# Kernel tuning notes

Hardware: AMD Instinct MI355X
Metric: run time of the kernel (lower is better)

## Reference

```python
import jax, jax.numpy as jnp
import numpy as np

N, DIM, HEADS, DHEAD = 4096, 1024, 16, 64
INNER = HEADS * DHEAD


def setup_inputs() -> dict:
    key = jax.random.key(0)
    ks = jax.random.split(key, 6)
    s_in = 1.0 / np.sqrt(DIM)
    s_inner = 1.0 / np.sqrt(INNER)
    return {
        "x": jax.random.normal(ks[0], (N, DIM), dtype=jnp.float32),
        # weights stored as (in, out) so y = x @ W
        "Wq": jax.random.uniform(ks[1], (DIM, INNER), jnp.float32, -s_in, s_in),
        "Wk": jax.random.uniform(ks[2], (DIM, INNER), jnp.float32, -s_in, s_in),
        "Wv": jax.random.uniform(ks[3], (DIM, INNER), jnp.float32, -s_in, s_in),
        "Wo": jax.random.uniform(ks[4], (INNER, DIM), jnp.float32, -s_inner, s_inner),
        "bo": jax.random.uniform(ks[5], (DIM,), jnp.float32, -s_inner, s_inner),
    }


def reference(x, Wq, Wk, Wv, Wo, bo):
    scale = DHEAD ** -0.5
    # [n, h, d] -> [h, n, d]
    q = (x @ Wq).reshape(N, HEADS, DHEAD).transpose(1, 0, 2)
    k = (x @ Wk).reshape(N, HEADS, DHEAD).transpose(1, 0, 2)
    v = (x @ Wv).reshape(N, HEADS, DHEAD).transpose(1, 0, 2)
    dots = jnp.einsum("hnd,hmd->hnm", q, k) * scale  # [h, n, n]
    attn = jax.nn.softmax(dots, axis=-1)
    out = jnp.einsum("hnm,hmd->hnd", attn, v)  # [h, n, d]
    out = out.transpose(1, 0, 2).reshape(N, INNER)
    return out @ Wo + bo
```

## Files before the change

kernel.cpp:

```cpp
#include <hip/hip_runtime.h>
#include <cstdint>
#include <cstddef>

typedef _Float16 f16;
typedef _Float16 f16x8 __attribute__((ext_vector_type(8)));
typedef _Float16 f16x4 __attribute__((ext_vector_type(4)));
typedef __fp16 fp16x2 __attribute__((ext_vector_type(2)));
typedef float floatx4 __attribute__((ext_vector_type(4)));
typedef float floatx16 __attribute__((ext_vector_type(16)));

constexpr int SEQ = 4096;
constexpr int DIM = 1024;
constexpr int NHEAD = 16;
constexpr int DH = 64;

#define QSCALE 0.18033688011112042f

__device__ __forceinline__ void async16(void* lds, const void* g) {
  __builtin_amdgcn_global_load_lds(
      (__attribute__((address_space(1))) void*)g,
      (__attribute__((address_space(3))) void*)lds, 16, 0, 0);
}

__device__ __forceinline__ uint32_t pk2(float a, float b) {
  union { fp16x2 h; uint32_t u; } c;
  c.h = __builtin_amdgcn_cvt_pkrtz(a, b);
  return c.u;
}

__device__ __forceinline__ float dot2acc(uint32_t packed, float acc) {
#if __has_builtin(__builtin_amdgcn_fdot2)
  union { uint32_t u; fp16x2 h; } c; c.u = packed;
  fp16x2 one2; one2.x = (__fp16)1.0f; one2.y = (__fp16)1.0f;
  return __builtin_amdgcn_fdot2(c.h, one2, acc, false);
#else
  union { uint32_t u; fp16x2 h; } c; c.u = packed;
  return acc + (float)c.h.x + (float)c.h.y;
#endif
}

__global__ void prep(const float* __restrict__ x, const float* __restrict__ w0,
                     const float* __restrict__ w1, const float* __restrict__ w2,
                     const float* __restrict__ w3, f16* __restrict__ xh,
                     f16* __restrict__ o0, f16* __restrict__ o1,
                     f16* __restrict__ o2, f16* __restrict__ o3) {
  int z = blockIdx.z;
  if (z == 4) {
    int blk = blockIdx.y * 32 + blockIdx.x;
    int tid = threadIdx.y * 32 + threadIdx.x;
    int base = (blk * 256 + tid) * 4;
#pragma unroll
    for (int c = 0; c < 4; ++c) {
      int i = base + c * (SEQ * DIM / 4);
      float4 v = *(const float4*)(x + i);
      f16x4 o;
      o.x = (f16)v.x; o.y = (f16)v.y; o.z = (f16)v.z; o.w = (f16)v.w;
      *(f16x4*)(xh + i) = o;
    }
    return;
  }
  __shared__ float tile[32][33];
  const float* W = (z == 0) ? w0 : (z == 1) ? w1 : (z == 2) ? w2 : w3;
  f16* O = (z == 0) ? o0 : (z == 1) ? o1 : (z == 2) ? o2 : o3;
  int tx = threadIdx.x, ty = threadIdx.y;
  int xc = blockIdx.x * 32 + tx;
  for (int i = ty; i < 32; i += 8)
    tile[i][tx] = W[(size_t)(blockIdx.y * 32 + i) * DIM + xc];
  __syncthreads();
  int xo = blockIdx.y * 32 + tx;
  for (int i = ty; i < 32; i += 8)
    O[(size_t)(blockIdx.x * 32 + i) * DIM + xo] = (f16)tile[tx][i];
}

__global__ __launch_bounds__(256, 2) void gemm_qkv(
    const f16* __restrict__ xh, const f16* __restrict__ wqt,
    const f16* __restrict__ wkt, const f16* __restrict__ wvt,
    f16* __restrict__ q_ws, f16* __restrict__ k_ws, f16* __restrict__ vt_ws) {
  __shared__ f16 smem[36864];
  const int tid = threadIdx.x;
  const int lane = tid & 63, l16 = lane & 15, quad = lane >> 4;
  const int w = tid >> 6, wr = w >> 1, wc = w & 1;
  const int m0 = blockIdx.x * 128, n0 = blockIdx.y * 256;
  const int z = blockIdx.z;
  const f16* Bt = (z == 0) ? wqt : (z == 1) ? wkt : wvt;

  floatx4 acc[4][8];
#pragma unroll
  for (int mt = 0; mt < 4; ++mt)
#pragma unroll
    for (int nt = 0; nt < 8; ++nt) acc[mt][nt] = (floatx4){0.f, 0.f, 0.f, 0.f};

#define QKV_STAGE(t_, buf_)                                                    \
  {                                                                            \
    int k0_ = (t_) * 32;                                                       \
    _Pragma("unroll")                                                          \
    for (int rnd = 0; rnd < 2; ++rnd) {                                        \
      int e = (rnd * 256 + tid) * 8;                                           \
      int cb = e >> 10, r = (e >> 3) & 127;                                    \
      async16((buf_) + e, xh + (size_t)(m0 + r) * DIM + k0_ + cb * 8);         \
    }                                                                          \
    _Pragma("unroll")                                                          \
    for (int rnd = 0; rnd < 4; ++rnd) {                                        \
      int e = (rnd * 256 + tid) * 8;                                           \
      int cb = e >> 11, r = (e >> 3) & 255;                                    \
      async16((buf_) + 4096 + e, Bt + (size_t)(n0 + r) * DIM + k0_ + cb * 8);  \
    }                                                                          \
  }

  QKV_STAGE(0, smem);
  QKV_STAGE(1, smem + 12288);
  for (int t = 0; t < 32; ++t) {
    f16* cur = smem + (t % 3) * 12288;
    if (t + 2 < 32) {
      QKV_STAGE(t + 2, smem + ((t + 2) % 3) * 12288);
      asm volatile("s_waitcnt vmcnt(12)" ::: "memory");
    } else if (t + 1 < 32) {
      asm volatile("s_waitcnt vmcnt(6)" ::: "memory");
    } else {
      asm volatile("s_waitcnt vmcnt(0)" ::: "memory");
    }
    __builtin_amdgcn_s_barrier();
    asm volatile("" ::: "memory");
    const f16* a_lds = cur;
    const f16* b_lds = cur + 4096;
    f16x8 af[4], bq[8];
#pragma unroll
    for (int mt = 0; mt < 4; ++mt)
      af[mt] = *(const f16x8*)(a_lds + quad * 1024 + (wr * 64 + mt * 16 + l16) * 8);
#pragma unroll
    for (int nt = 0; nt < 8; ++nt)
      bq[nt] = *(const f16x8*)(b_lds + quad * 2048 + (wc * 128 + nt * 16 + l16) * 8);
#pragma unroll
    for (int mt = 0; mt < 4; ++mt)
#pragma unroll
      for (int nt = 0; nt < 8; ++nt)
        acc[mt][nt] = __builtin_amdgcn_mfma_f32_16x16x32_f16(af[mt], bq[nt], acc[mt][nt], 0, 0, 0);
    asm volatile("" ::: "memory");
    __builtin_amdgcn_s_barrier();
  }
#undef QKV_STAGE

  if (z < 2) {
#pragma unroll
    for (int mt = 0; mt < 4; ++mt)
#pragma unroll
      for (int nt = 0; nt < 8; ++nt)
#pragma unroll
        for (int r = 0; r < 4; ++r) {
          int m = m0 + wr * 64 + mt * 16 + quad * 4 + r;
          int c = n0 + wc * 128 + nt * 16 + l16;
          float v = acc[mt][nt][r];
          if (z == 0)
            q_ws[(size_t)((c >> 6) * SEQ + m) * DH + (c & 63)] = (f16)(v * QSCALE);
          else
            k_ws[(size_t)((c >> 6) * SEQ + m) * DH + (c & 63)] = (f16)v;
        }
  } else {
#pragma unroll
    for (int ch = 0; ch < 2; ++ch) {
      if (wc == ch) {
#pragma unroll
        for (int mt = 0; mt < 4; ++mt)
#pragma unroll
          for (int nt = 0; nt < 8; ++nt)
#pragma unroll
            for (int r = 0; r < 4; ++r) {
              int cl = nt * 16 + l16;
              int ml = wr * 64 + mt * 16 + quad * 4 + r;
              smem[cl * 132 + ml] = (f16)acc[mt][nt][r];
            }
      }
      __syncthreads();
#pragma unroll
      for (int it = 0; it < 8; ++it) {
        int idx = it * 256 + tid;
        int cl = idx >> 4, mp = (idx & 15) * 8;
        f16x4 lo = *(const f16x4*)(smem + cl * 132 + mp);
        f16x4 hi4 = *(const f16x4*)(smem + cl * 132 + mp + 4);
        f16x8 v8;
#pragma unroll
        for (int j = 0; j < 4; ++j) { v8[j] = lo[j]; v8[4 + j] = hi4[j]; }
        *(f16x8*)(vt_ws + (size_t)(n0 + ch * 128 + cl) * SEQ + m0 + mp) = v8;
      }
      __syncthreads();
    }
  }
}

__global__ __launch_bounds__(256, 4) void attn_kernel(
    const f16* __restrict__ qg, const f16* __restrict__ kg,
    const f16* __restrict__ vtg, f16* __restrict__ og) {
  __shared__ f16 smem[16384];

  const int tid = threadIdx.x;
  const int w = tid >> 6, lane = tid & 63, l32 = lane & 31;
  const int hi = lane >> 5;

  const int pid = blockIdx.x + 32 * blockIdx.y;
  const int vid = (pid & 7) * 64 + (pid >> 3);
  const int qt = vid & 31, h = vid >> 5;

  const int q0 = qt * 128 + w * 32;

  f16x8 qf[4];
#pragma unroll
  for (int kf = 0; kf < 4; ++kf)
    qf[kf] = *(const f16x8*)(qg + (size_t)(h * SEQ + q0 + l32) * DH + kf * 16 + hi * 8);

  floatx16 oacc[2];
  oacc[0] = (floatx16)0.f; oacc[1] = (floatx16)0.f;
  float ssa = 0.f, ssb = 0.f;

  const f16* kg_h = kg + (size_t)h * SEQ * DH;
  const f16* vt_h = vtg + (size_t)h * DH * SEQ;
  constexpr int NT = SEQ / 64;

  {
#pragma unroll
    for (int rnd = 0; rnd < 2; ++rnd) {
      int e = (rnd * 256 + tid) * 8;
      int cb = e >> 9, r = (e >> 3) & 63;
      async16(smem + e, kg_h + (size_t)r * DH + cb * 8);
      async16(smem + 4096 + e, vt_h + (size_t)r * SEQ + cb * 8);
    }
  }

  for (int i = 0; i < NT; ++i) {
    f16* k_lds = smem + (i & 1) * 8192;
    f16* v_lds = k_lds + 4096;
    if (i + 1 < NT) {
      f16* kn = smem + ((i + 1) & 1) * 8192;
      const f16* ks = kg_h + (size_t)((i + 1) * 64) * DH;
      const f16* vs = vt_h + (i + 1) * 64;
#pragma unroll
      for (int rnd = 0; rnd < 2; ++rnd) {
        int e = (rnd * 256 + tid) * 8;
        int cb = e >> 9, r = (e >> 3) & 63;
        async16(kn + e, ks + (size_t)r * DH + cb * 8);
        async16(kn + 4096 + e, vs + (size_t)r * SEQ + cb * 8);
      }
      asm volatile("s_waitcnt vmcnt(4)" ::: "memory");
    } else {
      asm volatile("s_waitcnt vmcnt(0)" ::: "memory");
    }
    __builtin_amdgcn_s_barrier();
    asm volatile("" ::: "memory");

    floatx16 s0 = (floatx16)0.f, s1 = (floatx16)0.f;
    __builtin_amdgcn_s_setprio(1);
#pragma unroll
    for (int kf = 0; kf < 4; ++kf) {
      const f16* kr = k_lds + (kf * 2 + hi) * 512;
      f16x8 ka = *(const f16x8*)(kr + l32 * 8);
      f16x8 kc = *(const f16x8*)(kr + (32 + l32) * 8);
      s0 = __builtin_amdgcn_mfma_f32_32x32x16_f16(ka, qf[kf], s0, 0, 0, 0);
      s1 = __builtin_amdgcn_mfma_f32_32x32x16_f16(kc, qf[kf], s1, 0, 0, 0);
    }
    __builtin_amdgcn_s_setprio(0);

#pragma unroll
    for (int kb = 0; kb < 2; ++kb) {
      const floatx16 sacc = kb ? s1 : s0;
      f16x8 vf[2][2];
#pragma unroll
      for (int kh = 0; kh < 2; ++kh) {
        int cb = kb * 4 + kh * 2 + hi;
#pragma unroll
        for (int dt = 0; dt < 2; ++dt)
          vf[kh][dt] = *(const f16x8*)(v_lds + cb * 512 + (dt * 32 + l32) * 8);
      }
      float p[16];
#pragma unroll
      for (int r = 0; r < 16; ++r) p[r] = __builtin_amdgcn_exp2f(sacc[r]);
#pragma unroll
      for (int kh = 0; kh < 2; ++kh) {
        uint32_t d0a = pk2(p[8 * kh + 0], p[8 * kh + 1]);
        uint32_t d0b = pk2(p[8 * kh + 2], p[8 * kh + 3]);
        uint32_t d1a = pk2(p[8 * kh + 4], p[8 * kh + 5]);
        uint32_t d1b = pk2(p[8 * kh + 6], p[8 * kh + 7]);
        ssa = dot2acc(d0a, ssa);
        ssa = dot2acc(d0b, ssa);
        ssb = dot2acc(d1a, ssb);
        ssb = dot2acc(d1b, ssb);
        union { uint32_t u[4]; f16x8 v; } bu;
#if __has_builtin(__builtin_amdgcn_permlane32_swap)
        {
          auto sw1 = __builtin_amdgcn_permlane32_swap(d0a, d1a, false, false);
          auto sw2 = __builtin_amdgcn_permlane32_swap(d0b, d1b, false, false);
          bu.u[0] = sw1[0]; bu.u[1] = sw2[0]; bu.u[2] = sw1[1]; bu.u[3] = sw2[1];
        }
#else
        {
          uint32_t ra = (uint32_t)__shfl_xor((int)(hi ? d0a : d1a), 32);
          uint32_t rb = (uint32_t)__shfl_xor((int)(hi ? d0b : d1b), 32);
          bu.u[0] = hi ? ra : d0a;
          bu.u[1] = hi ? rb : d0b;
          bu.u[2] = hi ? d1a : ra;
          bu.u[3] = hi ? d1b : rb;
        }
#endif
        __builtin_amdgcn_s_setprio(1);
#pragma unroll
        for (int dt = 0; dt < 2; ++dt)
          oacc[dt] = __builtin_amdgcn_mfma_f32_32x32x16_f16(vf[kh][dt], bu.v, oacc[dt], 0, 0, 0);
        __builtin_amdgcn_s_setprio(0);
      }
    }
    asm volatile("" ::: "memory");
    __builtin_amdgcn_s_barrier();
    asm volatile("" ::: "memory");
  }

  float ssum = ssa + ssb;
  ssum += __shfl_xor(ssum, 32);
  float rn = 1.f / ssum;

  __syncthreads();
  f16* t = smem;
  const int ql = w * 32 + l32;
#pragma unroll
  for (int dt = 0; dt < 2; ++dt)
#pragma unroll
    for (int g = 0; g < 4; ++g) {
      f16x4 v4;
#pragma unroll
      for (int j = 0; j < 4; ++j) v4[j] = (f16)(oacc[dt][g * 4 + j] * rn);
      *(f16x4*)(t + ql * 68 + dt * 32 + 8 * g + 4 * hi) = v4;
    }
  __syncthreads();
#pragma unroll
  for (int it = 0; it < 4; ++it) {
    int idx = it * 256 + tid;
    int q = idx >> 3, dcol = (idx & 7) * 8;
    f16x4 lo = *(const f16x4*)(t + q * 68 + dcol);
    f16x4 hi4 = *(const f16x4*)(t + q * 68 + dcol + 4);
    f16x8 v8;
#pragma unroll
    for (int j = 0; j < 4; ++j) { v8[j] = lo[j]; v8[4 + j] = hi4[j]; }
    *(f16x8*)(og + (size_t)(qt * 128 + q) * DIM + h * DH + dcol) = v8;
  }
}

__global__ __launch_bounds__(256, 3) void gemm_o(
    const f16* __restrict__ ab, const f16* __restrict__ wot,
    const float* __restrict__ bo, float* __restrict__ out) {
  __shared__ f16 smem[16384];
  const int tid = threadIdx.x;
  const int lane = tid & 63, l16 = lane & 15, quad = lane >> 4;
  const int w = tid >> 6, wr = w >> 1, wc = w & 1;
  const int m0 = blockIdx.x * 128, n0 = blockIdx.y * 128;

  floatx4 acc[4][4];
#pragma unroll
  for (int mt = 0; mt < 4; ++mt)
#pragma unroll
    for (int nt = 0; nt < 4; ++nt) acc[mt][nt] = (floatx4){0.f, 0.f, 0.f, 0.f};

#define O_STAGE(t_, buf_)                                                      \
  {                                                                            \
    int k0_ = (t_) * 32;                                                       \
    _Pragma("unroll")                                                          \
    for (int rnd = 0; rnd < 2; ++rnd) {                                        \
      int e = (rnd * 256 + tid) * 8;                                           \
      int cb = e >> 10, r = (e >> 3) & 127;                                    \
      async16((buf_) + e, ab + (size_t)(m0 + r) * DIM + k0_ + cb * 8);         \
      async16((buf_) + 4096 + e, wot + (size_t)(n0 + r) * DIM + k0_ + cb * 8); \
    }                                                                          \
  }

  O_STAGE(0, smem);
  for (int t = 0; t < 32; ++t) {
    f16* cur = smem + (t & 1) * 8192;
    if (t + 1 < 32) {
      O_STAGE(t + 1, smem + ((t + 1) & 1) * 8192);
      asm volatile("s_waitcnt vmcnt(4)" ::: "memory");
    } else {
      asm volatile("s_waitcnt vmcnt(0)" ::: "memory");
    }
    __builtin_amdgcn_s_barrier();
    asm volatile("" ::: "memory");
    const f16* a_lds = cur;
    const f16* b_lds = cur + 4096;
    f16x8 af[4], bq[4];
#pragma unroll
    for (int mt = 0; mt < 4; ++mt)
      af[mt] = *(const f16x8*)(a_lds + quad * 1024 + (wr * 64 + mt * 16 + l16) * 8);
#pragma unroll
    for (int nt = 0; nt < 4; ++nt)
      bq[nt] = *(const f16x8*)(b_lds + quad * 1024 + (wc * 64 + nt * 16 + l16) * 8);
#pragma unroll
    for (int mt = 0; mt < 4; ++mt)
#pragma unroll
      for (int nt = 0; nt < 4; ++nt)
        acc[mt][nt] = __builtin_amdgcn_mfma_f32_16x16x32_f16(af[mt], bq[nt], acc[mt][nt], 0, 0, 0);
    asm volatile("" ::: "memory");
    __builtin_amdgcn_s_barrier();
  }
#undef O_STAGE

#pragma unroll
  for (int mt = 0; mt < 4; ++mt)
#pragma unroll
    for (int nt = 0; nt < 4; ++nt)
#pragma unroll
      for (int r = 0; r < 4; ++r) {
        int m = m0 + wr * 64 + mt * 16 + quad * 4 + r;
        int c = n0 + wc * 64 + nt * 16 + l16;
        out[(size_t)m * DIM + c] = acc[mt][nt][r] + bo[c];
      }
}


extern "C" void kernel_launch(void* const* d_in, const int* in_sizes, int n_in,
                              void* d_out, int out_size, void* d_ws, size_t ws_size,
                              hipStream_t stream) {
  (void)in_sizes; (void)n_in; (void)out_size; (void)ws_size;
  const float* x  = (const float*)d_in[0];
  const float* Wq = (const float*)d_in[1];
  const float* Wk = (const float*)d_in[2];
  const float* Wv = (const float*)d_in[3];
  const float* Wo = (const float*)d_in[4];
  const float* bo = (const float*)d_in[5];
  float* out = (float*)d_out;
  char* ws = (char*)d_ws;

  f16* xh    = (f16*)(ws);
  f16* wqt   = (f16*)(ws + (8u  << 20));
  f16* wkt   = (f16*)(ws + (10u << 20));
  f16* wvt   = (f16*)(ws + (12u << 20));
  f16* wot   = (f16*)(ws + (14u << 20));
  f16* q_ws  = (f16*)(ws + (16u << 20));
  f16* k_ws  = (f16*)(ws + (24u << 20));
  f16* vt_ws = (f16*)(ws + (32u << 20));
  f16* aout  = xh;

  prep<<<dim3(32, 32, 5), dim3(32, 8), 0, stream>>>(x, Wq, Wk, Wv, Wo, xh, wqt, wkt, wvt, wot);
  gemm_qkv<<<dim3(32, 4, 3), dim3(256), 0, stream>>>(xh, wqt, wkt, wvt, q_ws, k_ws, vt_ws);
  attn_kernel<<<dim3(SEQ / 128, NHEAD), dim3(256), 0, stream>>>(q_ws, k_ws, vt_ws, aout);
  gemm_o<<<dim3(32, 8), dim3(256), 0, stream>>>(aout, wot, bo, out);
}
```

Before: 243.8 us.

## Compute softmax row sums via MFMA with ones and stage Q/K/V epilogue stores

In the attention loop, the per-row softmax denominator is now accumulated by an extra 32x32x16 MFMA that multiplies a ones matrix with the packed probabilities. This replaces the VALU dot2 reductions and the final cross-half shuffle, but raises MFMA work by half per P·V step and adds 16 accumulator registers. In the QKV projection epilogue, Q/K tiles are now staged through LDS and written as 16-byte vectors instead of scattered scalar f16 stores. The V transpose is done in a single pass over both column halves rather than two passes with extra barriers, which needs more shared memory for the staging buffers.

Result: no change. 244.2 us (+0.2%).

```diff
diff --git a/kernel.cpp b/kernel.cpp
--- a/kernel.cpp
+++ b/kernel.cpp
@@ -26,17 +26,6 @@
   union { fp16x2 h; uint32_t u; } c;
   c.h = __builtin_amdgcn_cvt_pkrtz(a, b);
   return c.u;
-}
-
-__device__ __forceinline__ float dot2acc(uint32_t packed, float acc) {
-#if __has_builtin(__builtin_amdgcn_fdot2)
-  union { uint32_t u; fp16x2 h; } c; c.u = packed;
-  fp16x2 one2; one2.x = (__fp16)1.0f; one2.y = (__fp16)1.0f;
-  return __builtin_amdgcn_fdot2(c.h, one2, acc, false);
-#else
-  union { uint32_t u; fp16x2 h; } c; c.u = packed;
-  return acc + (float)c.h.x + (float)c.h.y;
-#endif
 }
 
 __global__ void prep(const float* __restrict__ x, const float* __restrict__ w0,
@@ -141,48 +130,49 @@
 #undef QKV_STAGE
 
   if (z < 2) {
+    f16* t = smem;
 #pragma unroll
     for (int mt = 0; mt < 4; ++mt)
 #pragma unroll
       for (int nt = 0; nt < 8; ++nt)
 #pragma unroll
         for (int r = 0; r < 4; ++r) {
-          int m = m0 + wr * 64 + mt * 16 + quad * 4 + r;
-          int c = n0 + wc * 128 + nt * 16 + l16;
+          int ml = wr * 64 + mt * 16 + quad * 4 + r;
+          int cl = wc * 128 + nt * 16 + l16;
           float v = acc[mt][nt][r];
-          if (z == 0)
-            q_ws[(size_t)((c >> 6) * SEQ + m) * DH + (c & 63)] = (f16)(v * QSCALE);
-          else
-            k_ws[(size_t)((c >> 6) * SEQ + m) * DH + (c & 63)] = (f16)v;
+          t[ml * 264 + cl] = (f16)((z == 0) ? v * QSCALE : v);
         }
+    __syncthreads();
+    f16* dst = (z == 0) ? q_ws : k_ws;
+#pragma unroll
+    for (int it = 0; it < 16; ++it) {
+      int idx = it * 256 + tid;
+      int m = idx >> 5, cc = (idx & 31) * 8;
+      f16x8 v8 = *(const f16x8*)(t + m * 264 + cc);
+      *(f16x8*)(dst + (size_t)(((n0 + cc) >> 6) * SEQ + m0 + m) * DH + (cc & 63)) = v8;
+    }
   } else {
 #pragma unroll
-    for (int ch = 0; ch < 2; ++ch) {
-      if (wc == ch) {
-#pragma unroll
-        for (int mt = 0; mt < 4; ++mt)
-#pragma unroll
-          for (int nt = 0; nt < 8; ++nt)
-#pragma unroll
-            for (int r = 0; r < 4; ++r) {
-              int cl = nt * 16 + l16;
-              int ml = wr * 64 + mt * 16 + quad * 4 + r;
-              smem[cl * 132 + ml] = (f16)acc[mt][nt][r];
-            }
-      }
-      __syncthreads();
-#pragma unroll
-      for (int it = 0; it < 8; ++it) {
-        int idx = it * 256 + tid;
-        int cl = idx >> 4, mp = (idx & 15) * 8;
-        f16x4 lo = *(const f16x4*)(smem + cl * 132 + mp);
-        f16x4 hi4 = *(const f16x4*)(smem + cl * 132 + mp + 4);
-        f16x8 v8;
-#pragma unroll
-        for (int j = 0; j < 4; ++j) { v8[j] = lo[j]; v8[4 + j] = hi4[j]; }
-        *(f16x8*)(vt_ws + (size_t)(n0 + ch * 128 + cl) * SEQ + m0 + mp) = v8;
-      }
-      __syncthreads();
+    for (int mt = 0; mt < 4; ++mt)
+#pragma unroll
+      for (int nt = 0; nt < 8; ++nt)
+#pragma unroll
+        for (int r = 0; r < 4; ++r) {
+          int cl = wc * 128 + nt * 16 + l16;
+          int ml = wr * 64 + mt * 16 + quad * 4 + r;
+          smem[cl * 132 + ml] = (f16)acc[mt][nt][r];
+        }
+    __syncthreads();
+#pragma unroll
+    for (int it = 0; it < 16; ++it) {
+      int idx = it * 256 + tid;
+      int cl = idx >> 4, mp = (idx & 15) * 8;
+      f16x4 lo = *(const f16x4*)(smem + cl * 132 + mp);
+      f16x4 hi4 = *(const f16x4*)(smem + cl * 132 + mp + 4);
+      f16x8 v8;
+#pragma unroll
+      for (int j = 0; j < 4; ++j) { v8[j] = lo[j]; v8[4 + j] = hi4[j]; }
+      *(f16x8*)(vt_ws + (size_t)(n0 + cl) * SEQ + m0 + mp) = v8;
     }
   }
 }
@@ -207,9 +197,13 @@
   for (int kf = 0; kf < 4; ++kf)
     qf[kf] = *(const f16x8*)(qg + (size_t)(h * SEQ + q0 + l32) * DH + kf * 16 + hi * 8);
 
+  f16x8 onesf;
+#pragma unroll
+  for (int j = 0; j < 8; ++j) onesf[j] = (f16)1.0f;
+
   floatx16 oacc[2];
   oacc[0] = (floatx16)0.f; oacc[1] = (floatx16)0.f;
-  float ssa = 0.f, ssb = 0.f;
+  floatx16 sext = (floatx16)0.f;
 
   const f16* kg_h = kg + (size_t)h * SEQ * DH;
   const f16* vt_h = vtg + (size_t)h * DH * SEQ;
@@ -278,10 +272,6 @@
         uint32_t d0b = pk2(p[8 * kh + 2], p[8 * kh + 3]);
         uint32_t d1a = pk2(p[8 * kh + 4], p[8 * kh + 5]);
         uint32_t d1b = pk2(p[8 * kh + 6], p[8 * kh + 7]);
-        ssa = dot2acc(d0a, ssa);
-        ssa = dot2acc(d0b, ssa);
-        ssb = dot2acc(d1a, ssb);
-        ssb = dot2acc(d1b, ssb);
         union { uint32_t u[4]; f16x8 v; } bu;
 #if __has_builtin(__builtin_amdgcn_permlane32_swap)
         {
@@ -300,6 +290,7 @@
         }
 #endif
         __builtin_amdgcn_s_setprio(1);
+        sext = __builtin_amdgcn_mfma_f32_32x32x16_f16(onesf, bu.v, sext, 0, 0, 0);
 #pragma unroll
         for (int dt = 0; dt < 2; ++dt)
           oacc[dt] = __builtin_amdgcn_mfma_f32_32x32x16_f16(vf[kh][dt], bu.v, oacc[dt], 0, 0, 0);
@@ -311,9 +302,7 @@
     asm volatile("" ::: "memory");
   }
 
-  float ssum = ssa + ssb;
-  ssum += __shfl_xor(ssum, 32);
-  float rn = 1.f / ssum;
+  float rn = 1.f / sext[0];
 
   __syncthreads();
   f16* t = smem;
```
